# Kernel optimization log

Hardware: AMD Instinct MI355X
Metric: run time of the kernel (lower is better)

## Reference

```python
import jax, jax.numpy as jnp
import numpy as np

B, S, D = 2, 2048, 2048
H, HK = 16, 4          # n_heads, n_kv_heads
DK = D // H            # 128
REP = H // HK


def setup_inputs() -> dict:
    key = jax.random.key(0)
    ks = jax.random.split(key, 9)
    x = jax.random.normal(ks[0], (B, S, D), dtype=jnp.float32)
    # RoPE tables: [max_seq_len, d_k/2]
    inv_freq = 1.0 / (10000.0 ** (jnp.arange(0, DK, 2, dtype=jnp.float32) / DK))
    t = jnp.arange(S, dtype=jnp.float32)
    freqs = jnp.outer(t, inv_freq)  # [S, DK/2]
    freqs_cos = jnp.cos(freqs)
    freqs_sin = jnp.sin(freqs)
    sc = 0.02
    return {
        "x": x,
        "freqs_cos": freqs_cos,
        "freqs_sin": freqs_sin,
        "wq_w": jax.random.normal(ks[1], (D, D), dtype=jnp.float32) * sc,
        "wq_b": jnp.zeros((D,), dtype=jnp.float32),
        "wk_w": jax.random.normal(ks[2], (HK * DK, D), dtype=jnp.float32) * sc,
        "wk_b": jnp.zeros((HK * DK,), dtype=jnp.float32),
        "wv_w": jax.random.normal(ks[3], (HK * DK, D), dtype=jnp.float32) * sc,
        "wv_b": jnp.zeros((HK * DK,), dtype=jnp.float32),
        "wo_w": jax.random.normal(ks[4], (D, D), dtype=jnp.float32) * sc,
        "wo_b": jnp.zeros((D,), dtype=jnp.float32),
    }


def _apply_rope(t, cos, sin):
    # t: [b, h, s, dk]; cos/sin: [1, 1, s, dk/2]; interleaved pairs (even=real, odd=imag)
    tr = t[..., 0::2]
    ti = t[..., 1::2]
    out_r = tr * cos - ti * sin
    out_i = tr * sin + ti * cos
    return jnp.stack([out_r, out_i], axis=-1).reshape(t.shape)


def reference(x, freqs_cos, freqs_sin, wq_w, wq_b, wk_w, wk_b, wv_w, wv_b, wo_w, wo_b):
    b, s, d = x.shape
    q = (x @ wq_w.T + wq_b).reshape(b, s, H, DK).transpose(0, 2, 1, 3)   # [b,H,s,dk]
    k = (x @ wk_w.T + wk_b).reshape(b, s, HK, DK).transpose(0, 2, 1, 3)  # [b,HK,s,dk]
    v = (x @ wv_w.T + wv_b).reshape(b, s, HK, DK).transpose(0, 2, 1, 3)

    cos = freqs_cos[:s][None, None]  # [1,1,s,dk/2]
    sin = freqs_sin[:s][None, None]
    q = _apply_rope(q, cos, sin)
    k = _apply_rope(k, cos, sin)

    # GQA: group q heads by kv head instead of materializing repeat_kv
    qg = q.reshape(b, HK, REP, s, DK)
    scores = jnp.einsum("bgrqd,bgkd->bgrqk", qg, k) / jnp.sqrt(jnp.float32(DK))
    causal = jnp.triu(jnp.full((s, s), -jnp.inf, dtype=scores.dtype), k=1)
    attn = jax.nn.softmax(scores + causal, axis=-1)  # dropout=0.0 -> no-op
    out = jnp.einsum("bgrqk,bgkd->bgrqd", attn, v)   # [b,HK,REP,s,dk]
    out = out.reshape(b, H, s, DK).transpose(0, 2, 1, 3).reshape(b, s, d)
    return out @ wo_w.T + wo_b
```

## Files before the change

kernel.cpp:

```cpp
#include <hip/hip_runtime.h>

#define BDIM 2
#define SDIM 2048
#define DDIM 2048
#define HQ 16
#define HKV 4
#define DKH 128
#define NKV 512
#define NQKV 3072
#define MROWS 4096

typedef __attribute__((ext_vector_type(8))) short bf16x8;
typedef __attribute__((ext_vector_type(4))) float f32x4;
typedef __attribute__((ext_vector_type(8))) unsigned short u16x8;
typedef __attribute__((ext_vector_type(4))) unsigned short u16x4;

#define AS1 __attribute__((address_space(1)))
#define AS3 __attribute__((address_space(3)))

__device__ __forceinline__ unsigned short f2bf(float f) {
    union { float f; unsigned int u; } v; v.f = f;
    unsigned int r = v.u + 0x7FFFu + ((v.u >> 16) & 1u);
    return (unsigned short)(r >> 16);
}
__device__ __forceinline__ float bf2f(unsigned short u) {
    union { unsigned int u; float f; } v; v.u = ((unsigned int)u) << 16;
    return v.f;
}
__device__ __forceinline__ unsigned int pack2bf(float a, float b) {
    return (unsigned int)f2bf(a) | ((unsigned int)f2bf(b) << 16);
}

#define NX   ((size_t)MROWS * DDIM)
#define NWQ  ((size_t)DDIM * DDIM)
#define NWKV ((size_t)NKV * DDIM)
__global__ void cast_all(const float* __restrict__ x, const float* __restrict__ wq,
                         const float* __restrict__ wk, const float* __restrict__ wv,
                         const float* __restrict__ wo, unsigned short* __restrict__ dst) {
    size_t i = ((size_t)blockIdx.x * blockDim.x + threadIdx.x) * 4;
    const size_t N0 = NX, N1 = N0 + NWQ, N2 = N1 + NWKV, N3 = N2 + NWKV, N4 = N3 + NWQ;
    if (i >= N4) return;
    const float* src; size_t off;
    if (i < N0)      { src = x;  off = i; }
    else if (i < N1) { src = wq; off = i - N0; }
    else if (i < N2) { src = wk; off = i - N1; }
    else if (i < N3) { src = wv; off = i - N2; }
    else             { src = wo; off = i - N3; }
    float4 v = *(const float4*)(src + off);
    u16x4 o;
    o[0] = f2bf(v.x); o[1] = f2bf(v.y); o[2] = f2bf(v.z); o[3] = f2bf(v.w);
    *(u16x4*)(dst + i) = o;
}

__global__ void concat_bias(const float* __restrict__ qb, const float* __restrict__ kb,
                            const float* __restrict__ vb, float* __restrict__ o) {
    int i = blockIdx.x * blockDim.x + threadIdx.x;
    if (i < DDIM) o[i] = qb[i];
    else if (i < DDIM + NKV) o[i] = kb[i - DDIM];
    else if (i < NQKV) o[i] = vb[i - DDIM - NKV];
}

__global__ void rope_v(unsigned short* __restrict__ buf,
                       const float* __restrict__ cosT, const float* __restrict__ sinT,
                       float qscale) {
    int r = blockIdx.x, pos = r & (SDIM - 1);
    int col0 = threadIdx.x * 8;
    unsigned short* p = buf + (size_t)r * NQKV + col0;
    int i0 = (col0 & 127) >> 1;
    float4 c4 = *(const float4*)(cosT + pos * 64 + i0);
    float4 s4 = *(const float4*)(sinT + pos * 64 + i0);
    float sc = (col0 < DDIM) ? qscale : 1.f;
    u16x8 v = *(const u16x8*)p;
    u16x8 o;
    float cc[4] = {c4.x, c4.y, c4.z, c4.w}, ss[4] = {s4.x, s4.y, s4.z, s4.w};
#pragma unroll
    for (int k = 0; k < 4; ++k) {
        float xr = bf2f(v[2 * k]), xi = bf2f(v[2 * k + 1]);
        o[2 * k]     = f2bf((xr * cc[k] - xi * ss[k]) * sc);
        o[2 * k + 1] = f2bf((xr * ss[k] + xi * cc[k]) * sc);
    }
    *(u16x8*)p = o;
}

__global__ void transpose_v(const unsigned short* __restrict__ qkv,
                            unsigned short* __restrict__ Vt) {
    __shared__ unsigned short T[32][33];
    int s0 = blockIdx.x * 32, d0 = blockIdx.y * 32, b = blockIdx.z;
    int c = threadIdx.x & 31, r4 = threadIdx.x >> 5;
    for (int rr = r4; rr < 32; rr += 8)
        T[rr][c] = qkv[(size_t)(b * SDIM + s0 + rr) * NQKV + (DDIM + NKV) + d0 + c];
    __syncthreads();
    int cp = ((c & 0x0C) << 1) | ((c & 0x10) >> 2) | (c & 3);
    for (int rr = r4; rr < 32; rr += 8)
        Vt[(size_t)(b * NKV + d0 + rr) * SDIM + s0 + cp] = T[c][rr];
}

template <int BF16OUT>
__global__ __launch_bounds__(256) void gemm_bt(
    const unsigned short* __restrict__ A,
    const unsigned short* __restrict__ Bm,
    const float* __restrict__ bias,
    void* __restrict__ Cv,
    int Ndim, int Kdim) {
    __shared__ unsigned short As[128 * 32];
    __shared__ unsigned short Bs[128 * 32];
    const int tid = threadIdx.x;
    const int w = tid >> 6, lane = tid & 63;
    const int ml = lane & 15, quad = lane >> 4;
    const int m0 = blockIdx.y * 128, n0 = blockIdx.x * 128;
    const int wr = (w >> 1) * 64, wc = (w & 1) * 64;

    f32x4 acc[4][4] = {};

    const int c0 = tid, c1 = tid + 256;
    const int ar0 = c0 >> 2, ak0 = (c0 & 3) * 8;
    const int ar1 = c1 >> 2, ak1 = (c1 & 3) * 8;

    for (int kt = 0; kt < Kdim; kt += 32) {
        __builtin_amdgcn_global_load_lds(
            (const AS1 unsigned int*)(A + (size_t)(m0 + ar0) * Kdim + kt + ak0),
            (AS3 unsigned int*)(As + c0 * 8), 16, 0, 0);
        __builtin_amdgcn_global_load_lds(
            (const AS1 unsigned int*)(A + (size_t)(m0 + ar1) * Kdim + kt + ak1),
            (AS3 unsigned int*)(As + c1 * 8), 16, 0, 0);
        __builtin_amdgcn_global_load_lds(
            (const AS1 unsigned int*)(Bm + (size_t)(n0 + ar0) * Kdim + kt + ak0),
            (AS3 unsigned int*)(Bs + c0 * 8), 16, 0, 0);
        __builtin_amdgcn_global_load_lds(
            (const AS1 unsigned int*)(Bm + (size_t)(n0 + ar1) * Kdim + kt + ak1),
            (AS3 unsigned int*)(Bs + c1 * 8), 16, 0, 0);
        __syncthreads();

        bf16x8 af[4], bfr[4];
#pragma unroll
        for (int i = 0; i < 4; ++i)
            af[i] = *(const bf16x8*)&As[(wr + i * 16 + ml) * 32 + quad * 8];
#pragma unroll
        for (int j = 0; j < 4; ++j)
            bfr[j] = *(const bf16x8*)&Bs[(wc + j * 16 + ml) * 32 + quad * 8];
#pragma unroll
        for (int i = 0; i < 4; ++i)
#pragma unroll
            for (int j = 0; j < 4; ++j)
                acc[i][j] = __builtin_amdgcn_mfma_f32_16x16x32_bf16(af[i], bfr[j], acc[i][j], 0, 0, 0);
        __syncthreads();
    }

#pragma unroll
    for (int j = 0; j < 4; ++j) {
        int col = n0 + wc + j * 16 + ml;
        float bj = bias[col];
#pragma unroll
        for (int i = 0; i < 4; ++i) {
            int row0 = m0 + wr + i * 16 + quad * 4;
#pragma unroll
            for (int r = 0; r < 4; ++r) {
                float v = acc[i][j][r] + bj;
                if (BF16OUT)
                    ((unsigned short*)Cv)[(size_t)(row0 + r) * Ndim + col] = f2bf(v);
                else
                    ((float*)Cv)[(size_t)(row0 + r) * Ndim + col] = v;
            }
        }
    }
}

__global__ __launch_bounds__(256, 2) void attn_fwd(
    const unsigned short* __restrict__ Qp,
    const unsigned short* __restrict__ Kp,
    const unsigned short* __restrict__ Vt,
    unsigned short* __restrict__ O) {
    const int l = blockIdx.x;
    const int qt = (l < 256) ? (15 - (l >> 5)) : ((l - 256) >> 5);
    const int h = l & 15;
    const int b = (l >> 4) & 1;
    const int g = h >> 2;
    const int tid = threadIdx.x;
    const int w = tid >> 6, lane = tid & 63;
    const int ml = lane & 15, quad = lane >> 4;
    const int seg = lane & 3, rsub = lane >> 2;

    __shared__ unsigned short Ks[4 * 64 * 32];
    __shared__ unsigned short Vs[2 * 128 * 32];

    bf16x8 aq[2][4];
#pragma unroll
    for (int g2 = 0; g2 < 2; ++g2) {
        const size_t qrow = (size_t)(b * SDIM + qt * 128 + w * 32 + g2 * 16 + ml);
#pragma unroll
        for (int kc = 0; kc < 4; ++kc)
            aq[g2][kc] = *(const bf16x8*)(Qp + qrow * NQKV + h * DKH + kc * 32 + quad * 8);
    }

    f32x4 o_acc[2][8] = {};
    float m_run[2] = {-INFINITY, -INFINITY}, l_run[2] = {0.f, 0.f};
    const int q0 = qt * 128 + w * 32;
    const int ktend = 2 * qt + 2;

    for (int kt = 0; kt < ktend; ++kt) {
        const int kb = kt * 64;
        __syncthreads();
#pragma unroll
        for (int kc = 0; kc < 4; ++kc)
            __builtin_amdgcn_global_load_lds(
                (const AS1 unsigned int*)(Kp + (size_t)(b * SDIM + kb + w * 16 + rsub) * NQKV + g * DKH + kc * 32 + seg * 8),
                (AS3 unsigned int*)(Ks + kc * 2048 + w * 512 + lane * 8), 16, 0, 0);
#pragma unroll
        for (int c = 0; c < 4; ++c) {
            int u = w * 4 + c, kc2 = u >> 3, rg = u & 7;
            __builtin_amdgcn_global_load_lds(
                (const AS1 unsigned int*)(Vt + (size_t)(b * NKV + g * DKH + rg * 16 + rsub) * SDIM + kb + kc2 * 32 + seg * 8),
                (AS3 unsigned int*)(Vs + u * 512 + lane * 8), 16, 0, 0);
        }
        __syncthreads();

        if (kb <= q0 + 31) {
            f32x4 st[2][4];
#pragma unroll
            for (int t = 0; t < 4; ++t) {
                bf16x8 ak[4];
#pragma unroll
                for (int kc = 0; kc < 4; ++kc)
                    ak[kc] = *(const bf16x8*)&Ks[kc * 2048 + (t * 16 + ml) * 32 + quad * 8];
#pragma unroll
                for (int g2 = 0; g2 < 2; ++g2) {
                    f32x4 sc = {};
#pragma unroll
                    for (int kc = 0; kc < 4; ++kc)
                        sc = __builtin_amdgcn_mfma_f32_16x16x32_bf16(ak[kc], aq[g2][kc], sc, 0, 0, 0);
                    st[g2][t] = sc;
                }
            }

            const bool diag = (kb + 63 > q0);
            float mx[2] = {-INFINITY, -INFINITY};
            if (diag) {
#pragma unroll
                for (int g2 = 0; g2 < 2; ++g2) {
                    int qg = q0 + g2 * 16 + ml;
#pragma unroll
                    for (int t = 0; t < 4; ++t) {
                        int kvb = kb + t * 16 + quad * 4;
#pragma unroll
                        for (int r = 0; r < 4; ++r) {
                            float x = st[g2][t][r];
                            if (kvb + r > qg) x = -INFINITY;
                            st[g2][t][r] = x;
                            mx[g2] = fmaxf(mx[g2], x);
                        }
                    }
                }
            } else {
#pragma unroll
                for (int g2 = 0; g2 < 2; ++g2)
#pragma unroll
                    for (int t = 0; t < 4; ++t)
#pragma unroll
                        for (int r = 0; r < 4; ++r)
                            mx[g2] = fmaxf(mx[g2], st[g2][t][r]);
            }
#pragma unroll
            for (int g2 = 0; g2 < 2; ++g2) {
                float m = mx[g2];
                m = fmaxf(m, __shfl_xor(m, 16));
                m = fmaxf(m, __shfl_xor(m, 32));
                float m_new = fmaxf(m_run[g2], m);
                float alpha = __expf(m_run[g2] - m_new);
                m_run[g2] = m_new;

                float lad = 0.f;
                unsigned int pk[4][2];
#pragma unroll
                for (int t = 0; t < 4; ++t) {
                    float p0 = __expf(st[g2][t][0] - m_new);
                    float p1 = __expf(st[g2][t][1] - m_new);
                    float p2 = __expf(st[g2][t][2] - m_new);
                    float p3 = __expf(st[g2][t][3] - m_new);
                    lad += (p0 + p1) + (p2 + p3);
                    pk[t][0] = pack2bf(p0, p1);
                    pk[t][1] = pack2bf(p2, p3);
                }
                lad += __shfl_xor(lad, 16);
                lad += __shfl_xor(lad, 32);
                l_run[g2] = l_run[g2] * alpha + lad;

#pragma unroll
                for (int dt = 0; dt < 8; ++dt)
#pragma unroll
                    for (int r = 0; r < 4; ++r)
                        o_acc[g2][dt][r] *= alpha;

#pragma unroll
                for (int c = 0; c < 2; ++c) {
                    union { unsigned int u[4]; bf16x8 v; } pb;
                    pb.u[0] = pk[2 * c][0];  pb.u[1] = pk[2 * c][1];
                    pb.u[2] = pk[2 * c + 1][0]; pb.u[3] = pk[2 * c + 1][1];
#pragma unroll
                    for (int dt = 0; dt < 8; ++dt) {
                        bf16x8 av = *(const bf16x8*)&Vs[c * 4096 + (dt * 16 + ml) * 32 + quad * 8];
                        o_acc[g2][dt] = __builtin_amdgcn_mfma_f32_16x16x32_bf16(av, pb.v, o_acc[g2][dt], 0, 0, 0);
                    }
                }
            }
        }
    }

#pragma unroll
    for (int g2 = 0; g2 < 2; ++g2) {
        float inv = 1.f / l_run[g2];
        size_t rowbase = (size_t)(b * SDIM + q0 + g2 * 16 + ml) * DDIM + h * DKH + quad * 4;
#pragma unroll
        for (int dt = 0; dt < 8; ++dt) {
            u16x4 ov;
#pragma unroll
            for (int r = 0; r < 4; ++r)
                ov[r] = f2bf(o_acc[g2][dt][r] * inv);
            *(u16x4*)(O + rowbase + dt * 16) = ov;
        }
    }
}

extern "C" void kernel_launch(void* const* d_in, const int* in_sizes, int n_in,
                              void* d_out, int out_size, void* d_ws, size_t ws_size,
                              hipStream_t stream) {
    const float* x    = (const float*)d_in[0];
    const float* fcos = (const float*)d_in[1];
    const float* fsin = (const float*)d_in[2];
    const float* wq_w = (const float*)d_in[3];
    const float* wq_b = (const float*)d_in[4];
    const float* wk_w = (const float*)d_in[5];
    const float* wk_b = (const float*)d_in[6];
    const float* wv_w = (const float*)d_in[7];
    const float* wv_b = (const float*)d_in[8];
    const float* wo_w = (const float*)d_in[9];
    const float* wo_b = (const float*)d_in[10];
    float* out = (float*)d_out;

    char* ws = (char*)d_ws;
    size_t off = 0;
    auto alloc = [&](size_t bytes) {
        char* p = ws + off;
        off += (bytes + 255) & ~(size_t)255;
        return p;
    };
    unsigned short* xb  = (unsigned short*)alloc(NX * 2);
    unsigned short* W3  = (unsigned short*)alloc((size_t)NQKV * DDIM * 2);
    unsigned short* wob = (unsigned short*)alloc(NWQ * 2);
    float* b3           = (float*)alloc((size_t)NQKV * 4);
    unsigned short* qkv = (unsigned short*)alloc((size_t)MROWS * NQKV * 2);
    unsigned short* Vt  = (unsigned short*)alloc((size_t)BDIM * NKV * SDIM * 2);
    unsigned short* att = (unsigned short*)alloc((size_t)MROWS * DDIM * 2);

    const size_t total4 = (NX + 2 * NWQ + 2 * NWKV) / 4;
    cast_all<<<dim3((unsigned)((total4 + 255) / 256)), dim3(256), 0, stream>>>(x, wq_w, wk_w, wv_w, wo_w, xb);
    concat_bias<<<dim3(12), dim3(256), 0, stream>>>(wq_b, wk_b, wv_b, b3);

    gemm_bt<1><<<dim3(NQKV / 128, MROWS / 128), 256, 0, stream>>>(xb, W3, b3, qkv, NQKV, DDIM);

    const float scale = 0.08838834764831845f;
    rope_v<<<dim3(MROWS), dim3(320), 0, stream>>>(qkv, fcos, fsin, scale);
    transpose_v<<<dim3(SDIM / 32, NKV / 32, BDIM), 256, 0, stream>>>(qkv, Vt);

    attn_fwd<<<dim3(512), dim3(256), 0, stream>>>(qkv, qkv + DDIM, Vt, att);

    gemm_bt<0><<<dim3(DDIM / 128, MROWS / 128), 256, 0, stream>>>(att, wob, wo_b, out, DDIM, DDIM);
}
```

Baseline: 334.4 us.

## Fuse V transpose into QKV GEMM epilogue and rebalance causal attention tiles

The QKV GEMM epilogue now writes the V columns straight into the transposed, permuted Vt layout. This removes the separate transpose kernel, and the qkv buffer shrinks to Q and K only (pitch 2560). The attention kernel pairs a short causal query tile with a long one inside each block (waves 0-1 take tile j, waves 2-3 take tile 31-j), so every block does similar work. It also skips rescaling the O accumulator when no row's max changed and interleaves the two row-group MFMAs to share V fragment loads. The risks are uncoalesced strided stores in the fused epilogue and a changed load balance across waves.

```diff
diff --git a/kernel.cpp b/kernel.cpp
--- a/kernel.cpp
+++ b/kernel.cpp
@@ -8,6 +8,7 @@
 #define DKH 128
 #define NKV 512
 #define NQKV 3072
+#define QKP 2560
 #define MROWS 4096
 
 typedef __attribute__((ext_vector_type(8))) short bf16x8;
@@ -65,7 +66,7 @@
                        float qscale) {
     int r = blockIdx.x, pos = r & (SDIM - 1);
     int col0 = threadIdx.x * 8;
-    unsigned short* p = buf + (size_t)r * NQKV + col0;
+    unsigned short* p = buf + (size_t)r * QKP + col0;
     int i0 = (col0 & 127) >> 1;
     float4 c4 = *(const float4*)(cosT + pos * 64 + i0);
     float4 s4 = *(const float4*)(sinT + pos * 64 + i0);
@@ -82,26 +83,14 @@
     *(u16x8*)p = o;
 }
 
-__global__ void transpose_v(const unsigned short* __restrict__ qkv,
-                            unsigned short* __restrict__ Vt) {
-    __shared__ unsigned short T[32][33];
-    int s0 = blockIdx.x * 32, d0 = blockIdx.y * 32, b = blockIdx.z;
-    int c = threadIdx.x & 31, r4 = threadIdx.x >> 5;
-    for (int rr = r4; rr < 32; rr += 8)
-        T[rr][c] = qkv[(size_t)(b * SDIM + s0 + rr) * NQKV + (DDIM + NKV) + d0 + c];
-    __syncthreads();
-    int cp = ((c & 0x0C) << 1) | ((c & 0x10) >> 2) | (c & 3);
-    for (int rr = r4; rr < 32; rr += 8)
-        Vt[(size_t)(b * NKV + d0 + rr) * SDIM + s0 + cp] = T[c][rr];
-}
-
-template <int BF16OUT>
+template <int MODE>
 __global__ __launch_bounds__(256) void gemm_bt(
     const unsigned short* __restrict__ A,
     const unsigned short* __restrict__ Bm,
     const float* __restrict__ bias,
     void* __restrict__ Cv,
-    int Ndim, int Kdim) {
+    unsigned short* __restrict__ VtOut,
+    int pitch, int Kdim) {
     __shared__ unsigned short As[128 * 32];
     __shared__ unsigned short Bs[128 * 32];
     const int tid = threadIdx.x;
@@ -146,20 +135,39 @@
         __syncthreads();
     }
 
-#pragma unroll
-    for (int j = 0; j < 4; ++j) {
-        int col = n0 + wc + j * 16 + ml;
-        float bj = bias[col];
-#pragma unroll
-        for (int i = 0; i < 4; ++i) {
-            int row0 = m0 + wr + i * 16 + quad * 4;
-#pragma unroll
-            for (int r = 0; r < 4; ++r) {
-                float v = acc[i][j][r] + bj;
-                if (BF16OUT)
-                    ((unsigned short*)Cv)[(size_t)(row0 + r) * Ndim + col] = f2bf(v);
-                else
-                    ((float*)Cv)[(size_t)(row0 + r) * Ndim + col] = v;
+    if (MODE == 1 && n0 >= 2560) {
+#pragma unroll
+        for (int j = 0; j < 4; ++j) {
+            int coln = n0 + wc + j * 16 + ml;
+            float bj = bias[coln];
+            int dg = coln - 2560;
+#pragma unroll
+            for (int i = 0; i < 4; ++i) {
+                int rowb = m0 + wr + i * 16;
+                int b_ = rowb >> 11;
+                int s_ = rowb & 2047;
+                u16x4 ov;
+#pragma unroll
+                for (int r = 0; r < 4; ++r) ov[r] = f2bf(acc[i][j][r] + bj);
+                *(u16x4*)(VtOut + (size_t)(b_ * NKV + dg) * SDIM + (s_ & ~31) + quad * 8 + (i & 1) * 4) = ov;
+            }
+        }
+    } else {
+#pragma unroll
+        for (int j = 0; j < 4; ++j) {
+            int col = n0 + wc + j * 16 + ml;
+            float bj = bias[col];
+#pragma unroll
+            for (int i = 0; i < 4; ++i) {
+                int row0 = m0 + wr + i * 16 + quad * 4;
+#pragma unroll
+                for (int r = 0; r < 4; ++r) {
+                    float v = acc[i][j][r] + bj;
+                    if (MODE == 1)
+                        ((unsigned short*)Cv)[(size_t)(row0 + r) * pitch + col] = f2bf(v);
+                    else
+                        ((float*)Cv)[(size_t)(row0 + r) * pitch + col] = v;
+                }
             }
         }
     }
@@ -171,7 +179,7 @@
     const unsigned short* __restrict__ Vt,
     unsigned short* __restrict__ O) {
     const int l = blockIdx.x;
-    const int qt = (l < 256) ? (15 - (l >> 5)) : ((l - 256) >> 5);
+    const int j = l >> 5;
     const int h = l & 15;
     const int b = (l >> 4) & 1;
     const int g = h >> 2;
@@ -183,19 +191,21 @@
     __shared__ unsigned short Ks[4 * 64 * 32];
     __shared__ unsigned short Vs[2 * 128 * 32];
 
+    const int myqt = (w < 2) ? j : (31 - j);
+    const int q0 = myqt * 64 + (w & 1) * 32;
+    const int ktend = 32 - j;
+
     bf16x8 aq[2][4];
 #pragma unroll
     for (int g2 = 0; g2 < 2; ++g2) {
-        const size_t qrow = (size_t)(b * SDIM + qt * 128 + w * 32 + g2 * 16 + ml);
+        const size_t qrow = (size_t)(b * SDIM + q0 + g2 * 16 + ml);
 #pragma unroll
         for (int kc = 0; kc < 4; ++kc)
-            aq[g2][kc] = *(const bf16x8*)(Qp + qrow * NQKV + h * DKH + kc * 32 + quad * 8);
+            aq[g2][kc] = *(const bf16x8*)(Qp + qrow * QKP + h * DKH + kc * 32 + quad * 8);
     }
 
     f32x4 o_acc[2][8] = {};
     float m_run[2] = {-INFINITY, -INFINITY}, l_run[2] = {0.f, 0.f};
-    const int q0 = qt * 128 + w * 32;
-    const int ktend = 2 * qt + 2;
 
     for (int kt = 0; kt < ktend; ++kt) {
         const int kb = kt * 64;
@@ -203,7 +213,7 @@
 #pragma unroll
         for (int kc = 0; kc < 4; ++kc)
             __builtin_amdgcn_global_load_lds(
-                (const AS1 unsigned int*)(Kp + (size_t)(b * SDIM + kb + w * 16 + rsub) * NQKV + g * DKH + kc * 32 + seg * 8),
+                (const AS1 unsigned int*)(Kp + (size_t)(b * SDIM + kb + w * 16 + rsub) * QKP + g * DKH + kc * 32 + seg * 8),
                 (AS3 unsigned int*)(Ks + kc * 2048 + w * 512 + lane * 8), 16, 0, 0);
 #pragma unroll
         for (int c = 0; c < 4; ++c) {
@@ -259,17 +269,21 @@
                         for (int r = 0; r < 4; ++r)
                             mx[g2] = fmaxf(mx[g2], st[g2][t][r]);
             }
+
+            float alpha[2];
+            unsigned int pk[2][4][2];
+            bool resc = false;
 #pragma unroll
             for (int g2 = 0; g2 < 2; ++g2) {
                 float m = mx[g2];
                 m = fmaxf(m, __shfl_xor(m, 16));
                 m = fmaxf(m, __shfl_xor(m, 32));
                 float m_new = fmaxf(m_run[g2], m);
-                float alpha = __expf(m_run[g2] - m_new);
+                resc = resc || (m_new > m_run[g2]);
+                alpha[g2] = __expf(m_run[g2] - m_new);
                 m_run[g2] = m_new;
 
                 float lad = 0.f;
-                unsigned int pk[4][2];
 #pragma unroll
                 for (int t = 0; t < 4; ++t) {
                     float p0 = __expf(st[g2][t][0] - m_new);
@@ -277,29 +291,37 @@
                     float p2 = __expf(st[g2][t][2] - m_new);
                     float p3 = __expf(st[g2][t][3] - m_new);
                     lad += (p0 + p1) + (p2 + p3);
-                    pk[t][0] = pack2bf(p0, p1);
-                    pk[t][1] = pack2bf(p2, p3);
+                    pk[g2][t][0] = pack2bf(p0, p1);
+                    pk[g2][t][1] = pack2bf(p2, p3);
                 }
                 lad += __shfl_xor(lad, 16);
                 lad += __shfl_xor(lad, 32);
-                l_run[g2] = l_run[g2] * alpha + lad;
-
-#pragma unroll
-                for (int dt = 0; dt < 8; ++dt)
-#pragma unroll
-                    for (int r = 0; r < 4; ++r)
-                        o_acc[g2][dt][r] *= alpha;
-
-#pragma unroll
-                for (int c = 0; c < 2; ++c) {
-                    union { unsigned int u[4]; bf16x8 v; } pb;
-                    pb.u[0] = pk[2 * c][0];  pb.u[1] = pk[2 * c][1];
-                    pb.u[2] = pk[2 * c + 1][0]; pb.u[3] = pk[2 * c + 1][1];
-#pragma unroll
-                    for (int dt = 0; dt < 8; ++dt) {
-                        bf16x8 av = *(const bf16x8*)&Vs[c * 4096 + (dt * 16 + ml) * 32 + quad * 8];
-                        o_acc[g2][dt] = __builtin_amdgcn_mfma_f32_16x16x32_bf16(av, pb.v, o_acc[g2][dt], 0, 0, 0);
-                    }
+                l_run[g2] = l_run[g2] * alpha[g2] + lad;
+            }
+
+            if (__ballot(resc)) {
+#pragma unroll
+                for (int g2 = 0; g2 < 2; ++g2)
+#pragma unroll
+                    for (int dt = 0; dt < 8; ++dt)
+#pragma unroll
+                        for (int r = 0; r < 4; ++r)
+                            o_acc[g2][dt][r] *= alpha[g2];
+            }
+
+#pragma unroll
+            for (int c = 0; c < 2; ++c) {
+                union { unsigned int u[4]; bf16x8 v; } pb[2];
+#pragma unroll
+                for (int g2 = 0; g2 < 2; ++g2) {
+                    pb[g2].u[0] = pk[g2][2 * c][0];     pb[g2].u[1] = pk[g2][2 * c][1];
+                    pb[g2].u[2] = pk[g2][2 * c + 1][0]; pb[g2].u[3] = pk[g2][2 * c + 1][1];
+                }
+#pragma unroll
+                for (int dt = 0; dt < 8; ++dt) {
+                    bf16x8 av = *(const bf16x8*)&Vs[c * 4096 + (dt * 16 + ml) * 32 + quad * 8];
+                    o_acc[0][dt] = __builtin_amdgcn_mfma_f32_16x16x32_bf16(av, pb[0].v, o_acc[0][dt], 0, 0, 0);
+                    o_acc[1][dt] = __builtin_amdgcn_mfma_f32_16x16x32_bf16(av, pb[1].v, o_acc[1][dt], 0, 0, 0);
                 }
             }
         }
@@ -347,7 +369,7 @@
     unsigned short* W3  = (unsigned short*)alloc((size_t)NQKV * DDIM * 2);
     unsigned short* wob = (unsigned short*)alloc(NWQ * 2);
     float* b3           = (float*)alloc((size_t)NQKV * 4);
-    unsigned short* qkv = (unsigned short*)alloc((size_t)MROWS * NQKV * 2);
+    unsigned short* qkv = (unsigned short*)alloc((size_t)MROWS * QKP * 2);
     unsigned short* Vt  = (unsigned short*)alloc((size_t)BDIM * NKV * SDIM * 2);
     unsigned short* att = (unsigned short*)alloc((size_t)MROWS * DDIM * 2);
 
@@ -355,13 +377,12 @@
     cast_all<<<dim3((unsigned)((total4 + 255) / 256)), dim3(256), 0, stream>>>(x, wq_w, wk_w, wv_w, wo_w, xb);
     concat_bias<<<dim3(12), dim3(256), 0, stream>>>(wq_b, wk_b, wv_b, b3);
 
-    gemm_bt<1><<<dim3(NQKV / 128, MROWS / 128), 256, 0, stream>>>(xb, W3, b3, qkv, NQKV, DDIM);
+    gemm_bt<1><<<dim3(NQKV / 128, MROWS / 128), 256, 0, stream>>>(xb, W3, b3, qkv, Vt, QKP, DDIM);
 
     const float scale = 0.08838834764831845f;
     rope_v<<<dim3(MROWS), dim3(320), 0, stream>>>(qkv, fcos, fsin, scale);
-    transpose_v<<<dim3(SDIM / 32, NKV / 32, BDIM), 256, 0, stream>>>(qkv, Vt);
 
     attn_fwd<<<dim3(512), dim3(256), 0, stream>>>(qkv, qkv + DDIM, Vt, att);
 
-    gemm_bt<0><<<dim3(DDIM / 128, MROWS / 128), 256, 0, stream>>>(att, wob, wo_b, out, DDIM, DDIM);
-}
+    gemm_bt<0><<<dim3(DDIM / 128, MROWS / 128), 256, 0, stream>>>(att, wob, wo_b, out, nullptr, DDIM, DDIM);
+}
```

New measurement: 359.7 us. 1.08x slower.

## Pair causal q-tiles per block, skip unneeded rescale, share V fragments

Applied to the files above, without the earlier changes.

Each attention block now serves two 64-row query tiles, a low one and its mirror high one, split across wave pairs, so every block has the same causal key-loop length and the load is balanced. The output rescale by alpha is skipped when no row max grew anywhere in the wave. The PV loop is reordered so each V fragment read from shared memory feeds both 16-row groups' MFMAs. The changed block-to-tile mapping and loop bound must still cover every query tile, and waves whose own tile ends early may still run the shared key loop, which needs correct masking of out-of-range keys.

```diff
diff --git a/kernel.cpp b/kernel.cpp
--- a/kernel.cpp
+++ b/kernel.cpp
@@ -101,7 +101,7 @@
     const unsigned short* __restrict__ Bm,
     const float* __restrict__ bias,
     void* __restrict__ Cv,
-    int Ndim, int Kdim) {
+    int pitch, int Kdim) {
     __shared__ unsigned short As[128 * 32];
     __shared__ unsigned short Bs[128 * 32];
     const int tid = threadIdx.x;
@@ -157,9 +157,9 @@
             for (int r = 0; r < 4; ++r) {
                 float v = acc[i][j][r] + bj;
                 if (BF16OUT)
-                    ((unsigned short*)Cv)[(size_t)(row0 + r) * Ndim + col] = f2bf(v);
+                    ((unsigned short*)Cv)[(size_t)(row0 + r) * pitch + col] = f2bf(v);
                 else
-                    ((float*)Cv)[(size_t)(row0 + r) * Ndim + col] = v;
+                    ((float*)Cv)[(size_t)(row0 + r) * pitch + col] = v;
             }
         }
     }
@@ -171,7 +171,7 @@
     const unsigned short* __restrict__ Vt,
     unsigned short* __restrict__ O) {
     const int l = blockIdx.x;
-    const int qt = (l < 256) ? (15 - (l >> 5)) : ((l - 256) >> 5);
+    const int j = l >> 5;
     const int h = l & 15;
     const int b = (l >> 4) & 1;
     const int g = h >> 2;
@@ -183,10 +183,15 @@
     __shared__ unsigned short Ks[4 * 64 * 32];
     __shared__ unsigned short Vs[2 * 128 * 32];
 
+    const bool low_pair = ((w < 2) != (l & 1));
+    const int myqt = low_pair ? j : (31 - j);
+    const int q0 = myqt * 64 + (w & 1) * 32;
+    const int ktend = 32 - j;
+
     bf16x8 aq[2][4];
 #pragma unroll
     for (int g2 = 0; g2 < 2; ++g2) {
-        const size_t qrow = (size_t)(b * SDIM + qt * 128 + w * 32 + g2 * 16 + ml);
+        const size_t qrow = (size_t)(b * SDIM + q0 + g2 * 16 + ml);
 #pragma unroll
         for (int kc = 0; kc < 4; ++kc)
             aq[g2][kc] = *(const bf16x8*)(Qp + qrow * NQKV + h * DKH + kc * 32 + quad * 8);
@@ -194,8 +199,6 @@
 
     f32x4 o_acc[2][8] = {};
     float m_run[2] = {-INFINITY, -INFINITY}, l_run[2] = {0.f, 0.f};
-    const int q0 = qt * 128 + w * 32;
-    const int ktend = 2 * qt + 2;
 
     for (int kt = 0; kt < ktend; ++kt) {
         const int kb = kt * 64;
@@ -259,17 +262,21 @@
                         for (int r = 0; r < 4; ++r)
                             mx[g2] = fmaxf(mx[g2], st[g2][t][r]);
             }
+
+            float alpha[2];
+            unsigned int pk[2][4][2];
+            bool resc = false;
 #pragma unroll
             for (int g2 = 0; g2 < 2; ++g2) {
                 float m = mx[g2];
                 m = fmaxf(m, __shfl_xor(m, 16));
                 m = fmaxf(m, __shfl_xor(m, 32));
                 float m_new = fmaxf(m_run[g2], m);
-                float alpha = __expf(m_run[g2] - m_new);
+                resc = resc || (m_new > m_run[g2]);
+                alpha[g2] = __expf(m_run[g2] - m_new);
                 m_run[g2] = m_new;
 
                 float lad = 0.f;
-                unsigned int pk[4][2];
 #pragma unroll
                 for (int t = 0; t < 4; ++t) {
                     float p0 = __expf(st[g2][t][0] - m_new);
@@ -277,29 +284,37 @@
                     float p2 = __expf(st[g2][t][2] - m_new);
                     float p3 = __expf(st[g2][t][3] - m_new);
                     lad += (p0 + p1) + (p2 + p3);
-                    pk[t][0] = pack2bf(p0, p1);
-                    pk[t][1] = pack2bf(p2, p3);
+                    pk[g2][t][0] = pack2bf(p0, p1);
+                    pk[g2][t][1] = pack2bf(p2, p3);
                 }
                 lad += __shfl_xor(lad, 16);
                 lad += __shfl_xor(lad, 32);
-                l_run[g2] = l_run[g2] * alpha + lad;
-
-#pragma unroll
-                for (int dt = 0; dt < 8; ++dt)
-#pragma unroll
-                    for (int r = 0; r < 4; ++r)
-                        o_acc[g2][dt][r] *= alpha;
-
-#pragma unroll
-                for (int c = 0; c < 2; ++c) {
-                    union { unsigned int u[4]; bf16x8 v; } pb;
-                    pb.u[0] = pk[2 * c][0];  pb.u[1] = pk[2 * c][1];
-                    pb.u[2] = pk[2 * c + 1][0]; pb.u[3] = pk[2 * c + 1][1];
-#pragma unroll
-                    for (int dt = 0; dt < 8; ++dt) {
-                        bf16x8 av = *(const bf16x8*)&Vs[c * 4096 + (dt * 16 + ml) * 32 + quad * 8];
-                        o_acc[g2][dt] = __builtin_amdgcn_mfma_f32_16x16x32_bf16(av, pb.v, o_acc[g2][dt], 0, 0, 0);
-                    }
+                l_run[g2] = l_run[g2] * alpha[g2] + lad;
+            }
+
+            if (__ballot(resc)) {
+#pragma unroll
+                for (int g2 = 0; g2 < 2; ++g2)
+#pragma unroll
+                    for (int dt = 0; dt < 8; ++dt)
+#pragma unroll
+                        for (int r = 0; r < 4; ++r)
+                            o_acc[g2][dt][r] *= alpha[g2];
+            }
+
+#pragma unroll
+            for (int c = 0; c < 2; ++c) {
+                union { unsigned int u[4]; bf16x8 v; } pb[2];
+#pragma unroll
+                for (int g2 = 0; g2 < 2; ++g2) {
+                    pb[g2].u[0] = pk[g2][2 * c][0];     pb[g2].u[1] = pk[g2][2 * c][1];
+                    pb[g2].u[2] = pk[g2][2 * c + 1][0]; pb[g2].u[3] = pk[g2][2 * c + 1][1];
+                }
+#pragma unroll
+                for (int dt = 0; dt < 8; ++dt) {
+                    bf16x8 av = *(const bf16x8*)&Vs[c * 4096 + (dt * 16 + ml) * 32 + quad * 8];
+                    o_acc[0][dt] = __builtin_amdgcn_mfma_f32_16x16x32_bf16(av, pb[0].v, o_acc[0][dt], 0, 0, 0);
+                    o_acc[1][dt] = __builtin_amdgcn_mfma_f32_16x16x32_bf16(av, pb[1].v, o_acc[1][dt], 0, 0, 0);
                 }
             }
         }
```

New measurement: 334.3 us. Within noise of the previous version (-0.1%).
